# Kernel optimization log

Hardware: AMD Instinct MI355X
Metric: run time of the kernel (lower is better)

The kernel has to match this reference:

```python
import jax, jax.numpy as jnp
import numpy as np


def setup_inputs() -> dict:
    key = jax.random.key(0)
    kq, kk, kv, km = jax.random.split(key, 4)
    B, H, N, D = 2, 16, 2048, 64
    q = jax.random.normal(kq, (B, H, N, D), dtype=jnp.float32)
    k = jax.random.normal(kk, (B, H, N, D), dtype=jnp.float32)
    v = jax.random.normal(kv, (B, H, N, D), dtype=jnp.float32)
    # mask > 0 means position is masked OUT (matches torch masked_fill(mask > 0, -max))
    mask = jax.random.randint(km, (B, N), 0, 2, dtype=jnp.int32)
    return {"q": q, "k": k, "v": v, "mask": mask}


def reference(q, k, v, mask):
    # q,k,v: [b,h,n,d]; mask: [b,j] with >0 = masked
    scale = q.shape[-1] ** -0.5
    sim = jnp.einsum('bhid,bhjd->bhij', q, k) * scale
    # l2_dist score modification: 2*qk*scale - ||q||^2 - ||k||^2
    q_sq = jnp.sum(q * q, axis=-1, keepdims=True)          # [b,h,i,1]
    k_sq = jnp.sum(k * k, axis=-1, keepdims=True)          # [b,h,j,1]
    sim = sim * 2 - q_sq - jnp.swapaxes(k_sq, -1, -2)       # [b,h,i,j]
    neg_max = -jnp.finfo(sim.dtype).max
    m = (mask > 0)[:, None, None, :]                        # [b,1,1,j]
    sim = jnp.where(m, neg_max, sim)
    attn = jax.nn.softmax(sim, axis=-1)
    out = jnp.einsum('bhij,bhjd->bhid', attn, v)
    return out
```

## Files before the change

kernel.cpp:

```cpp
#include <hip/hip_runtime.h>
#include <hip/hip_bf16.h>

#define NSEQ 2048
#define DD   64
#define HH   16
#define QT   128
#define KVB  64
#define NKV  (NSEQ / KVB)

typedef __attribute__((ext_vector_type(4)))  float f4;
typedef __attribute__((ext_vector_type(16))) float f32x16;
typedef __attribute__((ext_vector_type(8)))  short bf16x8;
typedef __attribute__((ext_vector_type(4)))  unsigned int u32x4;
typedef __attribute__((ext_vector_type(2)))  unsigned int u32x2;

#define QSCL  0.36067376022224085f
#define LOG2E 1.4426950408889634f
#define NEGBIG (-1.0e30f)

#define SWZ(row, q)  (((row) << 6) + ((((q) ^ ((row) & 7))) << 3))
#define SWZV(d, q)   (((d) << 6) + ((((q) ^ (((d) >> 2) & 7) ^ ((d) & 3))) << 3))

#if defined(__has_builtin)
#if __has_builtin(__builtin_amdgcn_exp2f)
#define EXP2F __builtin_amdgcn_exp2f
#endif
#if __has_builtin(__builtin_amdgcn_permlane32_swap)
#define HAVE_PLSWAP 1
#endif
#endif
#ifndef EXP2F
#define EXP2F exp2f
#endif

union bfu { u32x4 u; bf16x8 h; };

__device__ __forceinline__ unsigned cvtpk(float lo, float hi) {
    unsigned r;
    asm("v_cvt_pk_bf16_f32 %0, %1, %2" : "=v"(r) : "v"(lo), "v"(hi));
    return r;
}
template<int CTRL>
__device__ __forceinline__ float dppf(float x) {
    return __int_as_float(__builtin_amdgcn_update_dpp(
        0, __float_as_int(x), CTRL, 0xF, 0xF, true));
}
__device__ __forceinline__ float cross_add(float x) {
#ifdef HAVE_PLSWAP
    u32x2 r = __builtin_amdgcn_permlane32_swap(__float_as_uint(x), __float_as_uint(x),
                                               false, false);
    return __uint_as_float(r[0]) + __uint_as_float(r[1]);
#else
    return x + __shfl_xor(x, 32);
#endif
}
__device__ __forceinline__ void pairmix(unsigned A, unsigned B,
                                        unsigned& d0, unsigned& d2, bool hi) {
#ifdef HAVE_PLSWAP
    u32x2 r = __builtin_amdgcn_permlane32_swap(A, B, false, false);
    d0 = r[0]; d2 = r[1];
#else
    unsigned v = hi ? A : B;
    unsigned x = (unsigned)__shfl_xor((int)v, 32);
    d0 = hi ? x : A;
    d2 = hi ? B : x;
#endif
}

__global__ __launch_bounds__(256, 2)
void attend_kernel(const float* __restrict__ qg, const float* __restrict__ kg,
                   const float* __restrict__ vg, const int* __restrict__ maskg,
                   float* __restrict__ outg)
{
    __shared__ __align__(16) unsigned short Ks[2][KVB * DD];
    __shared__ __align__(16) unsigned short Vt[2][KVB * DD];
    __shared__ __align__(16) float bias_s[2][KVB];

    const int t    = threadIdx.x;
    const int w    = t >> 6;
    const int lane = t & 63;
    const int c5   = lane & 31;
    const int g2   = lane >> 5;

    const int p     = blockIdx.x;
    const int bh    = (p & 7) * 4 + ((p >> 3) >> 4);
    const int qtile = (p >> 3) & 15;
    const int b     = bh >> 4;

    const size_t base = (size_t)bh * NSEQ * DD;
    const float* kp = kg + base;
    const float* vp = vg + base;
    const int*   mp = maskg + b * NSEQ;

    bfu qf[4];
    {
        const float* qp = qg + base + (size_t)(qtile*QT + w*32 + c5) * DD;
        #pragma unroll
        for (int ck = 0; ck < 4; ++ck) {
            f4 a  = *(const f4*)(qp + ck*16 + g2*8);
            f4 bb = *(const f4*)(qp + ck*16 + g2*8 + 4);
            qf[ck].u = (u32x4){ cvtpk(a[0]*QSCL,  a[1]*QSCL),  cvtpk(a[2]*QSCL,  a[3]*QSCL),
                                cvtpk(bb[0]*QSCL, bb[1]*QSCL), cvtpk(bb[2]*QSCL, bb[3]*QSCL) };
        }
    }

    f32x16 acc0, acc1;
    #pragma unroll
    for (int r = 0; r < 16; ++r) { acc0[r] = 0.f; acc1[r] = 0.f; }
    float l_run = 0.f;

    const bool isK = (w < 2);
    const int  jK  = t >> 1;
    const int  kq0 = (t & 1) * 4;
    const int  uv  = t & 127;
    const int  dq  = uv & 15;
    const int  jq  = uv >> 4;

    f4  st[8];
    int mr = 0;

    auto loadTile = [&](int gt) {
        const int j0 = gt * KVB;
        if (isK) {
            const float* src = kp + (size_t)(j0 + jK) * DD + kq0 * 8;
            #pragma unroll
            for (int i2 = 0; i2 < 8; ++i2) st[i2] = ((const f4*)src)[i2];
            mr = mp[j0 + jK];
        } else {
            #pragma unroll
            for (int i2 = 0; i2 < 8; ++i2)
                st[i2] = *(const f4*)(vp + (size_t)(j0 + jq*8 + i2) * DD + dq*4);
        }
    };

    auto stageTile = [&](int bsel) {
        if (isK) {
            float sq = 0.f;
            #pragma unroll
            for (int i2 = 0; i2 < 8; ++i2)
                sq += st[i2][0]*st[i2][0] + st[i2][1]*st[i2][1]
                    + st[i2][2]*st[i2][2] + st[i2][3]*st[i2][3];
            sq += dppf<0xB1>(sq);
            if ((t & 1) == 0) bias_s[bsel][jK] = (mr > 0) ? NEGBIG : -sq * LOG2E;
            #pragma unroll
            for (int s2 = 0; s2 < 4; ++s2) {
                u32x4 kk = (u32x4){ cvtpk(st[2*s2][0],   st[2*s2][1]),
                                    cvtpk(st[2*s2][2],   st[2*s2][3]),
                                    cvtpk(st[2*s2+1][0], st[2*s2+1][1]),
                                    cvtpk(st[2*s2+1][2], st[2*s2+1][3]) };
                *(u32x4*)&Ks[bsel][SWZ(jK, kq0 + s2)] = kk;
            }
        } else {
            #pragma unroll
            for (int cc = 0; cc < 4; ++cc) {
                int d = dq*4 + cc;
                u32x4 tv = (u32x4){ cvtpk(st[0][cc], st[1][cc]),
                                    cvtpk(st[2][cc], st[3][cc]),
                                    cvtpk(st[4][cc], st[5][cc]),
                                    cvtpk(st[6][cc], st[7][cc]) };
                *(u32x4*)&Vt[bsel][SWZV(d, jq)] = tv;
            }
        }
    };

    loadTile(0);
    stageTile(0);
    loadTile(1);
    __syncthreads();

    int cur = 0;
    for (int kt = 0; kt < NKV; ++kt) {
        if (kt + 1 < NKV) stageTile(cur ^ 1);
        if (kt + 2 < NKV) loadTile(kt + 2);

        f32x16 s01[2];
        #pragma unroll
        for (int jt = 0; jt < 2; ++jt) {
            f4 b4[4];
            #pragma unroll
            for (int q = 0; q < 4; ++q)
                b4[q] = *(const f4*)&bias_s[cur][32*jt + 8*q + 4*g2];
            f32x16 sc;
            #pragma unroll
            for (int r = 0; r < 16; ++r) sc[r] = b4[r>>2][r&3];
            __builtin_amdgcn_s_setprio(1);
            #pragma unroll
            for (int ck = 0; ck < 4; ++ck) {
                bfu kb;
                kb.u = *(const u32x4*)&Ks[cur][SWZ(32*jt + c5, 2*ck + g2)];
                sc = __builtin_amdgcn_mfma_f32_32x32x16_bf16(kb.h, qf[ck].h, sc, 0, 0, 0);
            }
            __builtin_amdgcn_s_setprio(0);
            s01[jt] = sc;
        }

        unsigned Wp[16];
        float ls0 = 0.f, ls1 = 0.f;
        #pragma unroll
        for (int jt = 0; jt < 2; ++jt) {
            #pragma unroll
            for (int m = 0; m < 8; ++m) {
                float e0 = EXP2F(s01[jt][2*m]);
                float e1 = EXP2F(s01[jt][2*m+1]);
                if (m & 1) ls1 += e0 + e1; else ls0 += e0 + e1;
                Wp[jt*8 + m] = cvtpk(e0, e1);
            }
        }
        l_run += ls0 + ls1;

        const bool hi = (g2 != 0);
        __builtin_amdgcn_s_setprio(1);
        #pragma unroll
        for (int ck = 0; ck < 4; ++ck) {
            const int bs = (ck >> 1) * 8 + 4 * (ck & 1);
            unsigned d00, d20, d01, d21;
            pairmix(Wp[bs],   Wp[bs+2], d00, d20, hi);
            pairmix(Wp[bs+1], Wp[bs+3], d01, d21, hi);
            bfu pb;
            pb.u = (u32x4){ d00, d01, d20, d21 };
            bfu va0, va1;
            va0.u = *(const u32x4*)&Vt[cur][SWZV(     c5, 2*ck + g2)];
            va1.u = *(const u32x4*)&Vt[cur][SWZV(32 + c5, 2*ck + g2)];
            acc0 = __builtin_amdgcn_mfma_f32_32x32x16_bf16(va0.h, pb.h, acc0, 0, 0, 0);
            acc1 = __builtin_amdgcn_mfma_f32_32x32x16_bf16(va1.h, pb.h, acc1, 0, 0, 0);
        }
        __builtin_amdgcn_s_setprio(0);

        __syncthreads();
        cur ^= 1;
    }

    l_run = cross_add(l_run);
    float inv = 1.0f / l_run;
    float* op = outg + base + (size_t)(qtile*QT + w*32 + c5) * DD;
    #pragma unroll
    for (int dt = 0; dt < 2; ++dt) {
        const f32x16 A = dt ? acc1 : acc0;
        #pragma unroll
        for (int q = 0; q < 4; ++q) {
            f4 o = { A[4*q]*inv, A[4*q+1]*inv, A[4*q+2]*inv, A[4*q+3]*inv };
            *(f4*)(op + 32*dt + 8*q + 4*g2) = o;
        }
    }
}

extern "C" void kernel_launch(void* const* d_in, const int* in_sizes, int n_in,
                              void* d_out, int out_size, void* d_ws, size_t ws_size,
                              hipStream_t stream) {
    const float* q    = (const float*)d_in[0];
    const float* k    = (const float*)d_in[1];
    const float* v    = (const float*)d_in[2];
    const int*   mask = (const int*)d_in[3];
    float* out = (float*)d_out;
    attend_kernel<<<dim3(512), dim3(256), 0, stream>>>(q, k, v, mask, out);
}
```

Before: 56.23 us.

## Process two KV tiles per barrier with split accumulators

The main loop now handles two 64-row KV tiles per iteration, using doubled shared buffers and a single barrier per pair. Two independent output accumulator sets let the PV MFMA chains for each tile run without depending on each other, and they are summed at the end. Staging and global loads for the next pair are interleaved between the QK and PV phases. This halves the number of barriers and adds ILP, at the cost of twice the LDS (about 66KB per block, which may limit two blocks per CU) and more registers.

```diff
diff --git a/kernel.cpp b/kernel.cpp
--- a/kernel.cpp
+++ b/kernel.cpp
@@ -7,6 +7,7 @@
 #define QT   128
 #define KVB  64
 #define NKV  (NSEQ / KVB)
+#define NR   (NKV / 2)
 
 typedef __attribute__((ext_vector_type(4)))  float f4;
 typedef __attribute__((ext_vector_type(16))) float f32x16;
@@ -72,9 +73,9 @@
                    const float* __restrict__ vg, const int* __restrict__ maskg,
                    float* __restrict__ outg)
 {
-    __shared__ __align__(16) unsigned short Ks[2][KVB * DD];
-    __shared__ __align__(16) unsigned short Vt[2][KVB * DD];
-    __shared__ __align__(16) float bias_s[2][KVB];
+    __shared__ __align__(16) unsigned short Ks[2][2 * KVB * DD];
+    __shared__ __align__(16) unsigned short Vt[2][2 * KVB * DD];
+    __shared__ __align__(16) float bias_s[2][2 * KVB];
 
     const int t    = threadIdx.x;
     const int w    = t >> 6;
@@ -82,9 +83,9 @@
     const int c5   = lane & 31;
     const int g2   = lane >> 5;
 
-    const int p     = blockIdx.x;
-    const int bh    = (p & 7) * 4 + ((p >> 3) >> 4);
-    const int qtile = (p >> 3) & 15;
+    const int p0    = blockIdx.x;
+    const int bh    = (p0 & 7) * 4 + ((p0 >> 3) >> 4);
+    const int qtile = (p0 >> 3) & 15;
     const int b     = bh >> 4;
 
     const size_t base = (size_t)bh * NSEQ * DD;
@@ -104,9 +105,9 @@
         }
     }
 
-    f32x16 acc0, acc1;
+    f32x16 aA0, aA1, aB0, aB1;
     #pragma unroll
-    for (int r = 0; r < 16; ++r) { acc0[r] = 0.f; acc1[r] = 0.f; }
+    for (int r = 0; r < 16; ++r) { aA0[r]=0.f; aA1[r]=0.f; aB0[r]=0.f; aB1[r]=0.f; }
     float l_run = 0.f;
 
     const bool isK = (w < 2);
@@ -133,7 +134,7 @@
         }
     };
 
-    auto stageTile = [&](int bsel) {
+    auto stageTile = [&](int pbuf, int tsub) {
         if (isK) {
             float sq = 0.f;
             #pragma unroll
@@ -141,14 +142,14 @@
                 sq += st[i2][0]*st[i2][0] + st[i2][1]*st[i2][1]
                     + st[i2][2]*st[i2][2] + st[i2][3]*st[i2][3];
             sq += dppf<0xB1>(sq);
-            if ((t & 1) == 0) bias_s[bsel][jK] = (mr > 0) ? NEGBIG : -sq * LOG2E;
+            if ((t & 1) == 0) bias_s[pbuf][tsub*KVB + jK] = (mr > 0) ? NEGBIG : -sq * LOG2E;
             #pragma unroll
             for (int s2 = 0; s2 < 4; ++s2) {
                 u32x4 kk = (u32x4){ cvtpk(st[2*s2][0],   st[2*s2][1]),
                                     cvtpk(st[2*s2][2],   st[2*s2][3]),
                                     cvtpk(st[2*s2+1][0], st[2*s2+1][1]),
                                     cvtpk(st[2*s2+1][2], st[2*s2+1][3]) };
-                *(u32x4*)&Ks[bsel][SWZ(jK, kq0 + s2)] = kk;
+                *(u32x4*)&Ks[pbuf][tsub*(KVB*DD) + SWZ(jK, kq0 + s2)] = kk;
             }
         } else {
             #pragma unroll
@@ -158,43 +159,38 @@
                                     cvtpk(st[2][cc], st[3][cc]),
                                     cvtpk(st[4][cc], st[5][cc]),
                                     cvtpk(st[6][cc], st[7][cc]) };
-                *(u32x4*)&Vt[bsel][SWZV(d, jq)] = tv;
-            }
-        }
-    };
-
-    loadTile(0);
-    stageTile(0);
-    loadTile(1);
+                *(u32x4*)&Vt[pbuf][tsub*(KVB*DD) + SWZV(d, jq)] = tv;
+            }
+        }
+    };
+
+    loadTile(0); stageTile(0, 0);
+    loadTile(1); stageTile(0, 1);
+    loadTile(2);
     __syncthreads();
 
-    int cur = 0;
-    for (int kt = 0; kt < NKV; ++kt) {
-        if (kt + 1 < NKV) stageTile(cur ^ 1);
-        if (kt + 2 < NKV) loadTile(kt + 2);
-
-        f32x16 s01[2];
+    auto qkt = [&](int p, int tsub, f32x16* sOut) {
         #pragma unroll
         for (int jt = 0; jt < 2; ++jt) {
             f4 b4[4];
             #pragma unroll
             for (int q = 0; q < 4; ++q)
-                b4[q] = *(const f4*)&bias_s[cur][32*jt + 8*q + 4*g2];
+                b4[q] = *(const f4*)&bias_s[p][tsub*KVB + 32*jt + 8*q + 4*g2];
             f32x16 sc;
             #pragma unroll
-            for (int r = 0; r < 16; ++r) sc[r] = b4[r>>2][r&3];
+            for (int rr = 0; rr < 16; ++rr) sc[rr] = b4[rr>>2][rr&3];
             __builtin_amdgcn_s_setprio(1);
             #pragma unroll
             for (int ck = 0; ck < 4; ++ck) {
                 bfu kb;
-                kb.u = *(const u32x4*)&Ks[cur][SWZ(32*jt + c5, 2*ck + g2)];
+                kb.u = *(const u32x4*)&Ks[p][tsub*(KVB*DD) + SWZ(32*jt + c5, 2*ck + g2)];
                 sc = __builtin_amdgcn_mfma_f32_32x32x16_bf16(kb.h, qf[ck].h, sc, 0, 0, 0);
             }
             __builtin_amdgcn_s_setprio(0);
-            s01[jt] = sc;
-        }
-
-        unsigned Wp[16];
+            sOut[jt] = sc;
+        }
+    };
+    auto packP = [&](const f32x16* s01, unsigned* Wp) {
         float ls0 = 0.f, ls1 = 0.f;
         #pragma unroll
         for (int jt = 0; jt < 2; ++jt) {
@@ -207,8 +203,9 @@
             }
         }
         l_run += ls0 + ls1;
-
-        const bool hi = (g2 != 0);
+    };
+    const bool hi = (g2 != 0);
+    auto pv = [&](int p, int tsub, const unsigned* Wp, f32x16& o0, f32x16& o1) {
         __builtin_amdgcn_s_setprio(1);
         #pragma unroll
         for (int ck = 0; ck < 4; ++ck) {
@@ -219,15 +216,37 @@
             bfu pb;
             pb.u = (u32x4){ d00, d01, d20, d21 };
             bfu va0, va1;
-            va0.u = *(const u32x4*)&Vt[cur][SWZV(     c5, 2*ck + g2)];
-            va1.u = *(const u32x4*)&Vt[cur][SWZV(32 + c5, 2*ck + g2)];
-            acc0 = __builtin_amdgcn_mfma_f32_32x32x16_bf16(va0.h, pb.h, acc0, 0, 0, 0);
-            acc1 = __builtin_amdgcn_mfma_f32_32x32x16_bf16(va1.h, pb.h, acc1, 0, 0, 0);
+            va0.u = *(const u32x4*)&Vt[p][tsub*(KVB*DD) + SWZV(     c5, 2*ck + g2)];
+            va1.u = *(const u32x4*)&Vt[p][tsub*(KVB*DD) + SWZV(32 + c5, 2*ck + g2)];
+            o0 = __builtin_amdgcn_mfma_f32_32x32x16_bf16(va0.h, pb.h, o0, 0, 0, 0);
+            o1 = __builtin_amdgcn_mfma_f32_32x32x16_bf16(va1.h, pb.h, o1, 0, 0, 0);
         }
         __builtin_amdgcn_s_setprio(0);
+    };
+
+    for (int r = 0; r < NR; ++r) {
+        const int p = r & 1;
+
+        if (r + 1 < NR) { stageTile(p ^ 1, 0); loadTile(2*r + 3); }
+
+        unsigned WpA[16], WpB[16];
+        {
+            f32x16 sA[2];
+            qkt(p, 0, sA);
+            packP(sA, WpA);
+        }
+        {
+            f32x16 sB[2];
+            qkt(p, 1, sB);
+            packP(sB, WpB);
+        }
+
+        if (r + 1 < NR) { stageTile(p ^ 1, 1); if (r + 2 < NR) loadTile(2*r + 4); }
+
+        pv(p, 0, WpA, aA0, aA1);
+        pv(p, 1, WpB, aB0, aB1);
 
         __syncthreads();
-        cur ^= 1;
     }
 
     l_run = cross_add(l_run);
@@ -235,10 +254,12 @@
     float* op = outg + base + (size_t)(qtile*QT + w*32 + c5) * DD;
     #pragma unroll
     for (int dt = 0; dt < 2; ++dt) {
-        const f32x16 A = dt ? acc1 : acc0;
+        const f32x16 A = dt ? aA1 : aA0;
+        const f32x16 B = dt ? aB1 : aB0;
         #pragma unroll
         for (int q = 0; q < 4; ++q) {
-            f4 o = { A[4*q]*inv, A[4*q+1]*inv, A[4*q+2]*inv, A[4*q+3]*inv };
+            f4 o = { (A[4*q]  +B[4*q]  )*inv, (A[4*q+1]+B[4*q+1])*inv,
+                     (A[4*q+2]+B[4*q+2])*inv, (A[4*q+3]+B[4*q+3])*inv };
             *(f4*)(op + 32*dt + 8*q + 4*g2) = o;
         }
     }
```

Result: no change. 55.88 us (median of 2 runs) (-0.6%).
